# Optimization experiments

Hardware: AMD Instinct MI355X
Metric: run time of the kernel (lower is better)

The kernel has to match this reference:

```python
import jax, jax.numpy as jnp
import numpy as np
import math

L = 2          # num_layers
H = 1024       # hidden_dim
NH = 16        # num_heads
HD = H // NH   # head_dim = 64
M = 4096       # mlp_dim
GRIDS = [(2, 32, 32), (1, 32, 32)]  # (t,h,w) per image -> 2048 + 1024 = 3072 tokens
THETA = 10000.0
EPS = 1e-5


def _rope_cos_sin(grids, head_dim):
    # Rope2DPosEmbRepeated: interleaved (x,y) complex rotations, repeated over t.
    n = head_dim // 4
    freqs = 1.0 / (THETA ** (np.arange(0, head_dim, 4, dtype=np.float64)[:n] / head_dim))
    parts = []
    for t, h, w in grids:
        ys, xs = np.meshgrid(np.arange(h), np.arange(w), indexing='ij')
        xa = xs.reshape(-1, 1).astype(np.float64) * freqs  # [h*w, n]
        ya = ys.reshape(-1, 1).astype(np.float64) * freqs
        ang = np.stack([xa, ya], axis=-1).reshape(-1, head_dim // 2)  # interleave x,y
        parts.append(np.tile(ang, (t, 1)))
    ang = np.concatenate(parts, axis=0).astype(np.float32)  # [S, head_dim//2]
    return jnp.asarray(np.cos(ang)), jnp.asarray(np.sin(ang))


def _segment_ids(grids):
    lens = [t * h * w for t, h, w in grids]
    return jnp.asarray(np.repeat(np.arange(len(lens)), lens))


def _layernorm(x, g, b):
    mu = jnp.mean(x, axis=-1, keepdims=True)
    var = jnp.mean(jnp.square(x - mu), axis=-1, keepdims=True)
    return (x - mu) * jax.lax.rsqrt(var + EPS) * g + b


def _apply_rope(x, cos, sin):
    # x: [S, NH, HD]; cos/sin: [S, HD//2] -> broadcast over heads (unsqueeze(-2))
    xr = x.reshape(x.shape[0], x.shape[1], HD // 2, 2)
    a, b = xr[..., 0], xr[..., 1]
    c = cos[:, None, :]
    s = sin[:, None, :]
    oa = a * c - b * s
    ob = a * s + b * c
    return jnp.stack([oa, ob], axis=-1).reshape(x.shape)


def setup_inputs() -> dict:
    key = jax.random.key(0)
    ks = jax.random.split(key, 8)
    S = sum(t * h * w for t, h, w in GRIDS)
    sH = 1.0 / math.sqrt(H)
    sM = 1.0 / math.sqrt(M)
    return {
        'hidden_states': jax.random.normal(ks[0], (S, H), jnp.float32),
        'grid_thws': jnp.asarray(np.array(GRIDS, dtype=np.int32)),
        'ln0_g': jnp.ones((L, H), jnp.float32),
        'ln0_b': jnp.zeros((L, H), jnp.float32),
        'wqkv': jax.random.normal(ks[1], (L, 3 * H, H), jnp.float32) * sH,
        'wo': jax.random.normal(ks[2], (L, H, H), jnp.float32) * sH,
        'ln1_g': jnp.ones((L, H), jnp.float32),
        'ln1_b': jnp.zeros((L, H), jnp.float32),
        'fc0_w': jax.random.normal(ks[3], (L, M, H), jnp.float32) * math.sqrt(2.0 / H),
        'fc0_b': jnp.zeros((L, M), jnp.float32),
        'fc1_w': jax.random.normal(ks[4], (L, H, M), jnp.float32) * math.sqrt(2.0 / M),
        'fc1_b': jnp.zeros((L, H), jnp.float32),
        'fln_g': jnp.ones((H,), jnp.float32),
        'fln_b': jnp.zeros((H,), jnp.float32),
    }


def reference(hidden_states, grid_thws, ln0_g, ln0_b, wqkv, wo, ln1_g, ln1_b,
              fc0_w, fc0_b, fc1_w, fc1_b, fln_g, fln_b):
    grids = [tuple(int(v) for v in row) for row in np.asarray(grid_thws)]
    S = hidden_states.shape[0]
    cos, sin = _rope_cos_sin(grids, HD)
    seg = _segment_ids(grids)
    mask = seg[:, None] == seg[None, :]  # block-diagonal [S, S]
    scale = 1.0 / math.sqrt(HD)

    x = hidden_states
    for i in range(L):
        h = _layernorm(x, ln0_g[i], ln0_b[i])
        qkv = (h @ wqkv[i].T).reshape(S, 3, NH, HD)
        q, k, v = qkv[:, 0], qkv[:, 1], qkv[:, 2]
        q = _apply_rope(q, cos, sin)
        k = _apply_rope(k, cos, sin)
        scores = jnp.einsum('qhd,khd->hqk', q, k) * scale
        scores = jnp.where(mask[None], scores, -1e30)
        attn = jax.nn.softmax(scores, axis=-1)
        o = jnp.einsum('hqk,khd->qhd', attn, v).reshape(S, H)
        x = x + o @ wo[i].T
        h2 = _layernorm(x, ln1_g[i], ln1_b[i])
        mlp = jax.nn.gelu(h2 @ fc0_w[i].T + fc0_b[i], approximate=False) @ fc1_w[i].T + fc1_b[i]
        x = x + mlp
    return _layernorm(x, fln_g, fln_b)
```

## Files before the change

### kernel.cpp

```cpp
#include <hip/hip_runtime.h>
#include <hip/hip_bf16.h>
#include <cstdint>
#include <math.h>

constexpr int ST   = 3072;
constexpr int HH   = 1024;
constexpr int NHD  = 16;
constexpr int DH   = 64;
constexpr int MMLP = 4096;
constexpr int SEG0 = 2048;

using short8 = __attribute__((ext_vector_type(8))) short;
using f32x4  = __attribute__((ext_vector_type(4))) float;

#if __has_builtin(__builtin_amdgcn_exp2f)
#define EXP2F __builtin_amdgcn_exp2f
#else
#define EXP2F exp2f
#endif

#if __has_builtin(__builtin_amdgcn_rcpf)
#define RCPF __builtin_amdgcn_rcpf
#else
#define RCPF(x) (1.f / (x))
#endif

__device__ __forceinline__ unsigned short f2bf(float f) {
  unsigned int u = __float_as_uint(f);
  u += 0x7fffu + ((u >> 16) & 1u);
  return (unsigned short)(u >> 16);
}

__device__ __forceinline__ void g2l16(const void* g, void* l) {
  __builtin_amdgcn_global_load_lds(
      (const __attribute__((address_space(1))) unsigned int*)g,
      (__attribute__((address_space(3))) unsigned int*)l, 16, 0, 0);
}

__device__ __forceinline__ float erf_fast(float z) {
  const float az = fabsf(z);
  const float t1 = RCPF(1.f + 0.3275911f * az);
  const float poly =
      t1 * (0.254829592f +
            t1 * (-0.284496736f +
                  t1 * (1.421413741f +
                        t1 * (-1.453152027f + t1 * 1.061405429f))));
  const float e = EXP2F(-az * az * 1.4426950408889634f);
  const float v = 1.f - poly * e;
  return (z < 0.f) ? -v : v;
}

__global__ void cast_all(const float* __restrict__ s0,
                         const float* __restrict__ s1,
                         const float* __restrict__ s2,
                         const float* __restrict__ s3,
                         ushort4* __restrict__ dst) {
  const int i = blockIdx.x * blockDim.x + threadIdx.x;
  const float4* src;
  int off;
  if (i < 1572864)      { src = (const float4*)s0; off = i; }
  else if (i < 2097152) { src = (const float4*)s1; off = i - 1572864; }
  else if (i < 4194304) { src = (const float4*)s2; off = i - 2097152; }
  else                  { src = (const float4*)s3; off = i - 4194304; }
  const float4 v = src[off];
  ushort4 u;
  u.x = f2bf(v.x); u.y = f2bf(v.y); u.z = f2bf(v.z); u.w = f2bf(v.w);
  dst[i] = u;
}

__global__ void ln_kernel(const float* __restrict__ x,
                          const float* __restrict__ g,
                          const float* __restrict__ b,
                          unsigned short* obf) {
  const int s = blockIdx.x;
  const int t = threadIdx.x;
  const float4 v = ((const float4*)(x + (size_t)s * HH))[t];
  float s1 = v.x + v.y + v.z + v.w;
  float s2 = v.x * v.x + v.y * v.y + v.z * v.z + v.w * v.w;
#pragma unroll
  for (int off = 32; off > 0; off >>= 1) {
    s1 += __shfl_down(s1, off);
    s2 += __shfl_down(s2, off);
  }
  __shared__ float red[8];
  __shared__ float stat[2];
  const int wv = t >> 6, ln = t & 63;
  if (ln == 0) { red[wv] = s1; red[4 + wv] = s2; }
  __syncthreads();
  if (t == 0) {
    float a1 = red[0] + red[1] + red[2] + red[3];
    float a2 = red[4] + red[5] + red[6] + red[7];
    float mu = a1 * (1.f / HH);
    float var = a2 * (1.f / HH) - mu * mu;
    stat[0] = mu;
    stat[1] = rsqrtf(var + 1e-5f);
  }
  __syncthreads();
  const float mu = stat[0], rs = stat[1];
  const float4 gg = ((const float4*)g)[t];
  const float4 bb = ((const float4*)b)[t];
  ushort4 u;
  u.x = f2bf((v.x - mu) * rs * gg.x + bb.x);
  u.y = f2bf((v.y - mu) * rs * gg.y + bb.y);
  u.z = f2bf((v.z - mu) * rs * gg.z + bb.z);
  u.w = f2bf((v.w - mu) * rs * gg.w + bb.w);
  ((ushort4*)(obf + (size_t)s * HH))[t] = u;
}

template <int NS>
__global__ void ln_comb(const float* __restrict__ xin,
                        const float* __restrict__ P,
                        const float* __restrict__ bias,
                        const float* __restrict__ g,
                        const float* __restrict__ b,
                        float* __restrict__ xout,
                        unsigned short* obf, float* of) {
  const int s = blockIdx.x;
  const int t = threadIdx.x;
  const size_t row = (size_t)s * HH;
  const size_t sl = (size_t)ST * HH;
  float4 v = ((const float4*)(xin + row))[t];
#pragma unroll
  for (int c = 0; c < NS; ++c) {
    const float4 p = ((const float4*)(P + c * sl + row))[t];
    v.x += p.x; v.y += p.y; v.z += p.z; v.w += p.w;
  }
  if (bias) {
    const float4 bb4 = ((const float4*)bias)[t];
    v.x += bb4.x; v.y += bb4.y; v.z += bb4.z; v.w += bb4.w;
  }
  if (xout) ((float4*)(xout + row))[t] = v;
  float s1 = v.x + v.y + v.z + v.w;
  float s2 = v.x * v.x + v.y * v.y + v.z * v.z + v.w * v.w;
#pragma unroll
  for (int off = 32; off > 0; off >>= 1) {
    s1 += __shfl_down(s1, off);
    s2 += __shfl_down(s2, off);
  }
  __shared__ float red[8];
  __shared__ float stat[2];
  const int wv = t >> 6, ln = t & 63;
  if (ln == 0) { red[wv] = s1; red[4 + wv] = s2; }
  __syncthreads();
  if (t == 0) {
    float a1 = red[0] + red[1] + red[2] + red[3];
    float a2 = red[4] + red[5] + red[6] + red[7];
    float mu = a1 * (1.f / HH);
    float var = a2 * (1.f / HH) - mu * mu;
    stat[0] = mu;
    stat[1] = rsqrtf(var + 1e-5f);
  }
  __syncthreads();
  const float mu = stat[0], rs = stat[1];
  const float4 gg = ((const float4*)g)[t];
  const float4 bb = ((const float4*)b)[t];
  float4 o;
  o.x = (v.x - mu) * rs * gg.x + bb.x;
  o.y = (v.y - mu) * rs * gg.y + bb.y;
  o.z = (v.z - mu) * rs * gg.z + bb.z;
  o.w = (v.w - mu) * rs * gg.w + bb.w;
  if (obf) {
    ushort4 u;
    u.x = f2bf(o.x); u.y = f2bf(o.y); u.z = f2bf(o.z); u.w = f2bf(o.w);
    ((ushort4*)(obf + row))[t] = u;
  } else {
    ((float4*)(of + row))[t] = o;
  }
}

__global__ void rope_tables(float2* __restrict__ cs2) {
  const int s = blockIdx.x;
  const int j = threadIdx.x;
  const int p = (s < SEG0) ? (s & 1023) : (s - SEG0);
  const int pos = (j & 1) ? (p >> 5) : (p & 31);
  const int f = j >> 1;
  const double freq = pow(10000.0, -(double)f / 16.0);
  const double ang = (double)pos * freq;
  cs2[s * 32 + j] = make_float2((float)cos(ang), (float)sin(ang));
}

template <int MODE>
__launch_bounds__(256)
__global__ void gemm_bt(const unsigned short* __restrict__ A,
                        const unsigned short* __restrict__ B,
                        float* Cf, unsigned short* Cb,
                        const float* __restrict__ bias,
                        int N, int K) {
  __shared__ unsigned short Al[128 * 64];
  __shared__ unsigned short Bl[128 * 64];
  const int tid = threadIdx.x;
  const int lane = tid & 63;
  const int wave = tid >> 6;
  const int col = lane & 15;
  const int quad = lane >> 4;
  const int m0 = blockIdx.y * 128;
  const int n0 = blockIdx.x * 128;
  const int wm = (wave & 1) * 64;
  const int wn = (wave >> 1) * 64;

  int kFrom = 0, kTo = K;
  if (MODE == 4) {
    const int kc = K / gridDim.z;
    kFrom = blockIdx.z * kc;
    kTo = kFrom + kc;
  }

  f32x4 acc[4][4] = {};

  const int tr = tid >> 3;
  const int pb = tid & 7;
  const int kb = pb ^ (tr & 7);
  const unsigned short* Ag = A + (size_t)(m0 + tr) * K + kb * 8;
  const unsigned short* Bg = B + (size_t)(n0 + tr) * K + kb * 8;
  unsigned short* Alw = Al + (size_t)tid * 8;
  unsigned short* Blw = Bl + (size_t)tid * 8;

  for (int k0 = kFrom; k0 < kTo; k0 += 64) {
#pragma unroll
    for (int it = 0; it < 4; ++it) {
      g2l16(Ag + (size_t)(it * 32) * K + k0, Alw + it * 2048);
      g2l16(Bg + (size_t)(it * 32) * K + k0, Blw + it * 2048);
    }
    __syncthreads();
#pragma unroll
    for (int kk = 0; kk < 2; ++kk) {
      short8 af[4], bfr[4];
#pragma unroll
      for (int mt = 0; mt < 4; ++mt) {
        int r = wm + mt * 16 + col;
        int kp = (kk * 4 + quad) ^ (r & 7);
        af[mt] = *(const short8*)(Al + r * 64 + kp * 8);
      }
#pragma unroll
      for (int nt = 0; nt < 4; ++nt) {
        int r = wn + nt * 16 + col;
        int kp = (kk * 4 + quad) ^ (r & 7);
        bfr[nt] = *(const short8*)(Bl + r * 64 + kp * 8);
      }
#pragma unroll
      for (int mt = 0; mt < 4; ++mt)
#pragma unroll
        for (int nt = 0; nt < 4; ++nt)
          acc[mt][nt] = __builtin_amdgcn_mfma_f32_16x16x32_bf16(
              af[mt], bfr[nt], acc[mt][nt], 0, 0, 0);
    }
    __syncthreads();
  }

  if (MODE == 5) {
    const int bufsel = n0 >> 10;
    if (bufsel == 2) {
      unsigned short* vt = (unsigned short*)Cf;
#pragma unroll
      for (int mt = 0; mt < 4; ++mt) {
        const int gr0 = m0 + wm + mt * 16 + quad * 4;
#pragma unroll
        for (int nt = 0; nt < 4; ++nt) {
          const int gc = (n0 + wn + nt * 16 + col) & 1023;
          ushort4 u;
          u.x = f2bf(acc[mt][nt][0]);
          u.y = f2bf(acc[mt][nt][1]);
          u.z = f2bf(acc[mt][nt][2]);
          u.w = f2bf(acc[mt][nt][3]);
          *(ushort4*)(vt + (size_t)gc * ST + gr0) = u;
        }
      }
    } else {
      const float2* tab = (const float2*)bias;
      unsigned short* out = Cb + (size_t)bufsel * (ST * HH);
      const float SQ = 0.125f * 1.4426950408889634f;
#pragma unroll
      for (int mt = 0; mt < 4; ++mt) {
#pragma unroll
        for (int r = 0; r < 4; ++r) {
          const int gr = m0 + wm + mt * 16 + quad * 4 + r;
#pragma unroll
          for (int nt = 0; nt < 4; ++nt) {
            const int gc = n0 + wn + nt * 16 + col;
            const int c1023 = gc & 1023;
            const int j = (c1023 & 63) >> 1;
            const float2 cs = tab[gr * 32 + j];
            const float v = acc[mt][nt][r];
            const float vp = __shfl_xor(v, 1);
            float res = (lane & 1) ? (vp * cs.y + v * cs.x)
                                   : (v * cs.x - vp * cs.y);
            if (bufsel == 0) res *= SQ;
            const float rp = __shfl_xor(res, 1);
            if (!(lane & 1))
              *(unsigned int*)(out + (size_t)gr * HH + c1023) =
                  (unsigned)f2bf(res) | ((unsigned)f2bf(rp) << 16);
          }
        }
      }
    }
    return;
  }
  const size_t zoff = (MODE == 4) ? (size_t)blockIdx.z * ST * N : 0;
#pragma unroll
  for (int mt = 0; mt < 4; ++mt) {
#pragma unroll
    for (int r = 0; r < 4; ++r) {
      const int gr = m0 + wm + mt * 16 + quad * 4 + r;
#pragma unroll
      for (int nt = 0; nt < 4; ++nt) {
        const int gc = n0 + wn + nt * 16 + col;
        const float v = acc[mt][nt][r];
        if (MODE == 2) {
          const float tt = v + bias[gc];
          const float gl = 0.5f * tt * (1.f + erf_fast(tt * 0.70710678f));
          Cb[(size_t)gr * N + gc] = f2bf(gl);
        } else {
          Cf[zoff + (size_t)gr * N + gc] = v;
        }
      }
    }
  }
}

__launch_bounds__(256)
__global__ void attn_flash(const unsigned short* __restrict__ Qb,
                           const unsigned short* __restrict__ Kb,
                           const unsigned short* __restrict__ VT,
                           float* __restrict__ Op,
                           float* __restrict__ lbuf) {
  const int h = blockIdx.y;
  const int unit = blockIdx.x;
  int qt, chunk, s0;
  if (unit < 32) { qt = unit >> 1; chunk = unit & 1; s0 = 0; }
  else { qt = 16 + (unit - 32); chunk = 0; s0 = SEG0; }
  const int q0 = qt * 128;
  const int koff = s0 + chunk * 1024;

  const int tid = threadIdx.x;
  const int lane = tid & 63;
  const int wave = tid >> 6;
  const int col = lane & 15;
  const int quad = lane >> 4;

  __shared__ unsigned short Kl[128 * 64];
  __shared__ unsigned short Vl[64 * 128];
  __shared__ unsigned int Pl[4][2][2][16][20];

  short8 qf[2][2];
#pragma unroll
  for (int mt = 0; mt < 2; ++mt) {
    const unsigned short* qrow =
        Qb + (size_t)(q0 + wave * 32 + mt * 16 + col) * HH + h * DH;
    qf[mt][0] = *(const short8*)(qrow + quad * 8);
    qf[mt][1] = *(const short8*)(qrow + 32 + quad * 8);
  }

  short8 ones;
#pragma unroll
  for (int j = 0; j < 8; ++j) ones[j] = (short)0x3F80;

  f32x4 accO[2][4] = {};
  f32x4 accL[2] = {};
  const float SHIFT = 16.f;

  const int trK = tid >> 3, pbK = tid & 7;
  const int kbK = pbK ^ (trK & 7);
  const int trV = tid >> 4, pbV = tid & 15;

  for (int kb0 = 0; kb0 < 1024; kb0 += 128) {
#pragma unroll
    for (int it = 0; it < 4; ++it)
      g2l16(Kb + (size_t)(koff + kb0 + it * 32 + trK) * HH + h * DH + kbK * 8,
            (unsigned short*)Kl + it * 2048 + (size_t)tid * 8);
#pragma unroll
    for (int it = 0; it < 4; ++it) {
      const int d = it * 16 + trV;
      const int kbv = pbV ^ (d & 7);
      g2l16(VT + (size_t)(h * 64 + d) * ST + koff + kb0 + kbv * 8,
            (unsigned short*)Vl + it * 2048 + (size_t)tid * 8);
    }
    __syncthreads();

    f32x4 sc[2][8];
#pragma unroll
    for (int nt = 0; nt < 8; ++nt) {
      const int r = nt * 16 + col;
      const short8 kf0 = *(const short8*)(Kl + r * 64 + ((quad) ^ (r & 7)) * 8);
      const short8 kf1 = *(const short8*)(Kl + r * 64 + ((4 + quad) ^ (r & 7)) * 8);
#pragma unroll
      for (int mt = 0; mt < 2; ++mt) {
        f32x4 z = {};
        z = __builtin_amdgcn_mfma_f32_16x16x32_bf16(kf0, qf[mt][0], z, 0, 0, 0);
        sc[mt][nt] = __builtin_amdgcn_mfma_f32_16x16x32_bf16(kf1, qf[mt][1], z, 0, 0, 0);
      }
    }

#pragma unroll
    for (int kd = 0; kd < 4; ++kd) {
      const int par = kd & 1;
#pragma unroll
      for (int mt = 0; mt < 2; ++mt) {
#pragma unroll
        for (int ntl = 0; ntl < 2; ++ntl) {
          const f32x4 s4 = sc[mt][kd * 2 + ntl];
          const float p0 = EXP2F(s4[0] - SHIFT);
          const float p1 = EXP2F(s4[1] - SHIFT);
          const float p2 = EXP2F(s4[2] - SHIFT);
          const float p3 = EXP2F(s4[3] - SHIFT);
          uint2 w;
          w.x = (unsigned)f2bf(p0) | ((unsigned)f2bf(p1) << 16);
          w.y = (unsigned)f2bf(p2) | ((unsigned)f2bf(p3) << 16);
          *(uint2*)&Pl[wave][par][mt][col][ntl * 8 + quad * 2] = w;
        }
      }
      short8 pf[2];
#pragma unroll
      for (int mt = 0; mt < 2; ++mt)
        pf[mt] = *(const short8*)&Pl[wave][par][mt][col][quad * 4];
#pragma unroll
      for (int mt = 0; mt < 2; ++mt)
        accL[mt] = __builtin_amdgcn_mfma_f32_16x16x32_bf16(pf[mt], ones,
                                                           accL[mt], 0, 0, 0);
#pragma unroll
      for (int dt = 0; dt < 4; ++dt) {
        const int rv = dt * 16 + col;
        const int pbv2 = (kd * 4 + quad) ^ (rv & 7);
        const short8 vf = *(const short8*)(Vl + rv * 128 + pbv2 * 8);
#pragma unroll
        for (int mt = 0; mt < 2; ++mt)
          accO[mt][dt] = __builtin_amdgcn_mfma_f32_16x16x32_bf16(
              pf[mt], vf, accO[mt][dt], 0, 0, 0);
      }
    }
    __syncthreads();
  }

  float* Opc = Op + (size_t)chunk * (ST * HH);
#pragma unroll
  for (int mt = 0; mt < 2; ++mt)
#pragma unroll
    for (int r = 0; r < 4; ++r) {
      const int row = q0 + wave * 32 + mt * 16 + quad * 4 + r;
#pragma unroll
      for (int dt = 0; dt < 4; ++dt)
        Opc[(size_t)row * HH + h * DH + dt * 16 + col] = accO[mt][dt][r];
      if (col == 0)
        lbuf[((size_t)chunk * ST + row) * NHD + h] = accL[mt][r];
    }
}

__global__ void attn_combine(const float* __restrict__ Op,
                             const float* __restrict__ lbuf,
                             unsigned short* __restrict__ out) {
  const int s = blockIdx.x;
  const int t = threadIdx.x;
  const int h = t >> 4;
  const int d0 = (t & 15) * 4;
  const int nc = (s < SEG0) ? 2 : 1;
  float L = 0.f;
  float4 o = make_float4(0.f, 0.f, 0.f, 0.f);
  for (int c = 0; c < nc; ++c) {
    L += lbuf[((size_t)c * ST + s) * NHD + h];
    const float4 v =
        *(const float4*)(Op + (size_t)c * (ST * HH) + (size_t)s * HH + h * DH + d0);
    o.x += v.x; o.y += v.y; o.z += v.z; o.w += v.w;
  }
  const float inv = 1.f / L;
  ushort4 u;
  u.x = f2bf(o.x * inv); u.y = f2bf(o.y * inv);
  u.z = f2bf(o.z * inv); u.w = f2bf(o.w * inv);
  ((ushort4*)(out + (size_t)s * HH))[t] = u;
}

extern "C" void kernel_launch(void* const* d_in, const int* in_sizes, int n_in,
                              void* d_out, int out_size, void* d_ws, size_t ws_size,
                              hipStream_t stream) {
  const float* hs   = (const float*)d_in[0];
  const float* ln0g = (const float*)d_in[2];
  const float* ln0b = (const float*)d_in[3];
  const float* wqkv = (const float*)d_in[4];
  const float* wo   = (const float*)d_in[5];
  const float* ln1g = (const float*)d_in[6];
  const float* ln1b = (const float*)d_in[7];
  const float* fc0w = (const float*)d_in[8];
  const float* fc0b = (const float*)d_in[9];
  const float* fc1w = (const float*)d_in[10];
  const float* fc1b = (const float*)d_in[11];
  const float* fln_g = (const float*)d_in[12];
  const float* fln_b = (const float*)d_in[13];

  char* ws = (char*)d_ws;
  unsigned short* wqkv_bf = (unsigned short*)(ws + 0);
  unsigned short* wo_bf   = (unsigned short*)(ws + 12582912);
  unsigned short* fc0_bf  = (unsigned short*)(ws + 16777216);
  unsigned short* fc1_bf  = (unsigned short*)(ws + 33554432);
  float*          x       = (float*)(ws + 50331648);
  unsigned short* abf     = (unsigned short*)(ws + 62914560);
  unsigned short* gelu_bf = (unsigned short*)(ws + 69206016);
  unsigned short* Qbf     = (unsigned short*)(ws + 132120576);
  unsigned short* Kbf     = (unsigned short*)(ws + 138412032);
  float*          cs2tab  = (float*)(ws + 150994944);
  unsigned short* VT    = (unsigned short*)(ws + 94371840);
  float*          Op    = (float*)(ws + 100663296);
  float*          lbuf  = (float*)(ws + 144703488);
  float*          Pbuf  = (float*)(ws + 94371840);

  cast_all<<<24576, 256, 0, stream>>>(wqkv, wo, fc0w, fc1w, (ushort4*)ws);
  rope_tables<<<ST, 32, 0, stream>>>((float2*)cs2tab);

  for (int i = 0; i < 2; ++i) {
    if (i == 0)
      ln_kernel<<<ST, 256, 0, stream>>>(hs, ln0g, ln0b, abf);
    gemm_bt<5><<<dim3(24, 24), 256, 0, stream>>>(
        abf, wqkv_bf + (size_t)i * 3 * HH * HH, (float*)VT, Qbf, cs2tab,
        3 * HH, HH);
    attn_flash<<<dim3(40, 16), 256, 0, stream>>>(Qbf, Kbf, VT, Op, lbuf);
    attn_combine<<<ST, 256, 0, stream>>>(Op, lbuf, abf);
    gemm_bt<4><<<dim3(8, 24, 2), 256, 0, stream>>>(
        abf, wo_bf + (size_t)i * HH * HH, Pbuf, nullptr, nullptr, HH, HH);
    ln_comb<2><<<ST, 256, 0, stream>>>(
        (i == 0) ? hs : x, Pbuf, nullptr, ln1g + i * HH, ln1b + i * HH,
        x, abf, nullptr);
    gemm_bt<2><<<dim3(32, 24), 256, 0, stream>>>(
        abf, fc0_bf + (size_t)i * MMLP * HH, nullptr, gelu_bf, fc0b + i * MMLP,
        MMLP, HH);
    gemm_bt<4><<<dim3(8, 24, 2), 256, 0, stream>>>(
        gelu_bf, fc1_bf + (size_t)i * HH * MMLP, Pbuf, nullptr, nullptr,
        HH, MMLP);
    if (i == 0)
      ln_comb<2><<<ST, 256, 0, stream>>>(x, Pbuf, fc1b, ln0g + HH, ln0b + HH,
                                         x, abf, nullptr);
    else
      ln_comb<2><<<ST, 256, 0, stream>>>(x, Pbuf, fc1b + HH, fln_g, fln_b,
                                         nullptr, nullptr, (float*)d_out);
  }
}
```

Baseline: 618.9 us.

## Store split-K partials as bf16 and transpose V through LDS for coalesced stores

Split-K GEMM partial outputs (out-proj and fc1) are now written as bf16 instead of fp32, and the residual/LayerNorm combine kernel reads them as packed bf16. This halves the partial-sum traffic on both the write and the read side. Separately, the V-transpose epilogue of the QKV GEMM stages the tile in LDS with a swizzle and then writes 16-byte row chunks, replacing scattered 8-byte stores. Rounding the partials to bf16 before summation costs some accuracy in the residual stream.

```diff
diff --git a/kernel.cpp b/kernel.cpp
--- a/kernel.cpp
+++ b/kernel.cpp
@@ -29,6 +29,13 @@
   unsigned int u = __float_as_uint(f);
   u += 0x7fffu + ((u >> 16) & 1u);
   return (unsigned short)(u >> 16);
+}
+
+__device__ __forceinline__ float bf2f_lo(unsigned int u) {
+  return __uint_as_float(u << 16);
+}
+__device__ __forceinline__ float bf2f_hi(unsigned int u) {
+  return __uint_as_float(u & 0xffff0000u);
 }
 
 __device__ __forceinline__ void g2l16(const void* g, void* l) {
@@ -109,7 +116,7 @@
 
 template <int NS>
 __global__ void ln_comb(const float* __restrict__ xin,
-                        const float* __restrict__ P,
+                        const unsigned short* __restrict__ Pb,
                         const float* __restrict__ bias,
                         const float* __restrict__ g,
                         const float* __restrict__ b,
@@ -122,8 +129,9 @@
   float4 v = ((const float4*)(xin + row))[t];
 #pragma unroll
   for (int c = 0; c < NS; ++c) {
-    const float4 p = ((const float4*)(P + c * sl + row))[t];
-    v.x += p.x; v.y += p.y; v.z += p.z; v.w += p.w;
+    const uint2 p = ((const uint2*)(Pb + c * sl + row))[t];
+    v.x += bf2f_lo(p.x); v.y += bf2f_hi(p.x);
+    v.z += bf2f_lo(p.y); v.w += bf2f_hi(p.y);
   }
   if (bias) {
     const float4 bb4 = ((const float4*)bias)[t];
@@ -186,8 +194,9 @@
                         float* Cf, unsigned short* Cb,
                         const float* __restrict__ bias,
                         int N, int K) {
-  __shared__ unsigned short Al[128 * 64];
-  __shared__ unsigned short Bl[128 * 64];
+  __shared__ unsigned short Sl[16384];
+  unsigned short* Al = Sl;
+  unsigned short* Bl = Sl + 8192;
   const int tid = threadIdx.x;
   const int lane = tid & 63;
   const int wave = tid >> 6;
@@ -250,20 +259,34 @@
   if (MODE == 5) {
     const int bufsel = n0 >> 10;
     if (bufsel == 2) {
+      unsigned int* T32 = (unsigned int*)Sl;
+#pragma unroll
+      for (int mt = 0; mt < 4; ++mt) {
+        const int d0 = (wm + mt * 16 + quad * 4) >> 1;
+#pragma unroll
+        for (int nt = 0; nt < 4; ++nt) {
+          const int cl = wn + nt * 16 + col;
+          const int swz = (cl & 7) << 3;
+          uint2 w;
+          w.x = (unsigned)f2bf(acc[mt][nt][0]) |
+                ((unsigned)f2bf(acc[mt][nt][1]) << 16);
+          w.y = (unsigned)f2bf(acc[mt][nt][2]) |
+                ((unsigned)f2bf(acc[mt][nt][3]) << 16);
+          *(uint2*)&T32[cl * 64 + (d0 ^ swz)] = w;
+        }
+      }
+      __syncthreads();
       unsigned short* vt = (unsigned short*)Cf;
-#pragma unroll
-      for (int mt = 0; mt < 4; ++mt) {
-        const int gr0 = m0 + wm + mt * 16 + quad * 4;
-#pragma unroll
-        for (int nt = 0; nt < 4; ++nt) {
-          const int gc = (n0 + wn + nt * 16 + col) & 1023;
-          ushort4 u;
-          u.x = f2bf(acc[mt][nt][0]);
-          u.y = f2bf(acc[mt][nt][1]);
-          u.z = f2bf(acc[mt][nt][2]);
-          u.w = f2bf(acc[mt][nt][3]);
-          *(ushort4*)(vt + (size_t)gc * ST + gr0) = u;
-        }
+      const int cl = tid >> 1;
+      const int half = tid & 1;
+      const int swz = (cl & 7) << 3;
+      const int gch = (n0 & 1023) + cl;
+      unsigned short* dst = vt + (size_t)gch * ST + m0 + half * 64;
+#pragma unroll
+      for (int j4 = 0; j4 < 8; ++j4) {
+        const int d = half * 32 + j4 * 4;
+        const uint4 v4 = *(const uint4*)&T32[cl * 64 + (d ^ swz)];
+        *(uint4*)(dst + j4 * 8) = v4;
       }
     } else {
       const float2* tab = (const float2*)bias;
@@ -310,7 +333,7 @@
           const float gl = 0.5f * tt * (1.f + erf_fast(tt * 0.70710678f));
           Cb[(size_t)gr * N + gc] = f2bf(gl);
         } else {
-          Cf[zoff + (size_t)gr * N + gc] = v;
+          Cb[zoff + (size_t)gr * N + gc] = f2bf(v);
         }
       }
     }
@@ -498,7 +521,7 @@
   unsigned short* VT    = (unsigned short*)(ws + 94371840);
   float*          Op    = (float*)(ws + 100663296);
   float*          lbuf  = (float*)(ws + 144703488);
-  float*          Pbuf  = (float*)(ws + 94371840);
+  unsigned short* Pbuf  = (unsigned short*)(ws + 94371840);
 
   cast_all<<<24576, 256, 0, stream>>>(wqkv, wo, fc0w, fc1w, (ushort4*)ws);
   rope_tables<<<ST, 32, 0, stream>>>((float2*)cs2tab);
@@ -512,7 +535,7 @@
     attn_flash<<<dim3(40, 16), 256, 0, stream>>>(Qbf, Kbf, VT, Op, lbuf);
     attn_combine<<<ST, 256, 0, stream>>>(Op, lbuf, abf);
     gemm_bt<4><<<dim3(8, 24, 2), 256, 0, stream>>>(
-        abf, wo_bf + (size_t)i * HH * HH, Pbuf, nullptr, nullptr, HH, HH);
+        abf, wo_bf + (size_t)i * HH * HH, nullptr, Pbuf, nullptr, HH, HH);
     ln_comb<2><<<ST, 256, 0, stream>>>(
         (i == 0) ? hs : x, Pbuf, nullptr, ln1g + i * HH, ln1b + i * HH,
         x, abf, nullptr);
@@ -520,7 +543,7 @@
         abf, fc0_bf + (size_t)i * MMLP * HH, nullptr, gelu_bf, fc0b + i * MMLP,
         MMLP, HH);
     gemm_bt<4><<<dim3(8, 24, 2), 256, 0, stream>>>(
-        gelu_bf, fc1_bf + (size_t)i * HH * MMLP, Pbuf, nullptr, nullptr,
+        gelu_bf, fc1_bf + (size_t)i * HH * MMLP, nullptr, Pbuf, nullptr,
         HH, MMLP);
     if (i == 0)
       ln_comb<2><<<ST, 256, 0, stream>>>(x, Pbuf, fc1b, ln0g + HH, ln0b + HH,
```

Measured after the change: 612.2 us. No clear change (-1.1%).
